# Kernel tuning notes

Hardware: AMD Instinct MI355X
Metric: run time of the kernel (lower is better)

## Reference

```python
import jax, jax.numpy as jnp
import numpy as np
from jax import lax

# Dimensions: B=batch, C=in_channels(=shells, shallow deep=0), O=out_channels,
# G=12 group orientations, (X,Y,Z)=volume, (H,W)=icosahedral chart plane.
B, C, O, G = 1, 8, 8, 12
X = 12
CH, CW = 8, 40  # chart height H and width 5*H (5 charts)


def setup_inputs() -> dict:
    key = jax.random.key(0)
    k1, k2, k3, k4 = jax.random.split(key, 4)
    x = jax.random.normal(k1, (B, C, X, X, X, CH, CW), jnp.float32)
    weight = 0.1 * jax.random.normal(k2, (O, C, 3, 3, 3, 7), jnp.float32)
    bias = 0.1 * jax.random.normal(k3, (O, 3, 3, 3), jnp.float32)
    # d12.basis_expansion (detached constant): 7 hex coeffs -> 12 oriented 3x3 kernels
    basis_e_h = jax.random.normal(k4, (G, 7, 3, 3), jnp.float32)
    # d12.padding_basis(H): chart-padding index maps. Interior = identity;
    # border ring gathers from adjacent-chart interior with orientation permutation.
    ys = jnp.arange(CH)
    xs = jnp.arange(CW)
    I = jnp.broadcast_to(jnp.clip(ys, 1, CH - 2)[:, None], (CH, CW)).astype(jnp.int32)
    J = jnp.broadcast_to(jnp.clip(xs, 1, CW - 2)[None, :], (CH, CW)).astype(jnp.int32)
    border = (ys[:, None] == 0) | (ys[:, None] == CH - 1) | (xs[None, :] == 0) | (xs[None, :] == CW - 1)
    g = jnp.arange(G)[:, None, None]
    T = jnp.where(border[None], (g + 1) % G, g).astype(jnp.int32)
    # d12.bias_basis: broadcast O biases over 12 orientations (g-major channel layout)
    bias_basis = jnp.tile(jnp.arange(O), G).astype(jnp.int32)
    return dict(x=x, weight=weight, bias=bias, basis_e_h=basis_e_h, I=I, J=J, T=T, bias_basis=bias_basis)


def _forward(x, weight, bias, basis_e_h, I, J, T, bias_basis):
    B, C, X, Y, Z, H, W = x.shape
    O = weight.shape[0]
    G = basis_e_h.shape[0]
    GO = G * O
    # Expand symmetry basis: per 3x3x3 offset, a [G*O, C, 3, 3] 2D kernel.
    kernel = jnp.einsum('ocijkb,gbuv->gocijkuv', weight, basis_e_h).reshape(GO, C, 3, 3, 3, 3, 3)
    # Original fills out[i+1] for i in range(X-3): Xo = X-3 valid positions (drops last).
    Xo, Yo, Zo = X - 3, Y - 3, Z - 3
    dn = ('NCHW', 'OIHW', 'NCHW')
    N = B * Xo * Yo * Zo
    acc = jnp.zeros((N, GO, H - 2, W - 2), x.dtype)
    # Sum over the 27 kernel offsets; each is a valid 3x3 conv2d on the chart plane.
    for fi in range(3):
        for fj in range(3):
            for fk in range(3):
                xs_ = x[:, :, fi:fi + Xo, fj:fj + Yo, fk:fk + Zo]  # [B,C,Xo,Yo,Zo,H,W]
                xs2 = xs_.transpose(0, 2, 3, 4, 1, 5, 6).reshape(N, C, H, W)
                acc = acc + lax.conv_general_dilated(xs2, kernel[:, :, fi, fj, fk], (1, 1), 'VALID', dimension_numbers=dn)
    # Sum of per-offset biases (bias added inside conv2d, before zero-pad ring).
    acc = acc + bias.sum(axis=(1, 2, 3))[bias_basis][None, :, None, None]
    acc = jnp.pad(acc, ((0, 0), (0, 0), (1, 1), (1, 1)))  # F.pad (1,1,1,1) -> [N,GO,H,W]
    # d12.pad: fill chart ring by gather with orientation permutation T.
    P = acc.reshape(N, G, O, H, W).transpose(0, 2, 1, 3, 4)  # [N,O,G,H,W]
    Ib = jnp.broadcast_to(I[None], (G, H, W))
    Jb = jnp.broadcast_to(J[None], (G, H, W))
    Pp = P[:, :, T, Ib, Jb]  # [N,O,G,H,W]
    res = Pp.transpose(0, 2, 1, 3, 4).reshape(B, Xo, Yo, Zo, GO, H, W).transpose(0, 4, 1, 2, 3, 5, 6)
    # Scatter into zero-initialized full volume at positions 1..X-3.
    out = jnp.zeros((B, GO, X, Y, Z, H, W), x.dtype)
    return out.at[:, :, 1:1 + Xo, 1:1 + Yo, 1:1 + Zo].set(res)


def reference(x, weight, bias, basis_e_h, I, J, T, bias_basis):
    return _forward(x, weight, bias, basis_e_h, I, J, T, bias_basis)
```

## Files before the change

### kernel.cpp

```cpp
#include <hip/hip_runtime.h>


#define HW 320
#define NZ 3
#define NPAD 1944

__global__ __launch_bounds__(320, 8) void fused_kernel(
    const float* __restrict__ x, const float* __restrict__ weight,
    const float* __restrict__ bias, const float* __restrict__ basis,
    float* __restrict__ out)
{
    __shared__ float qs[NZ * 7 * HW];

    const int tid = threadIdx.x;

    {
        float4* out4 = (float4*)out;
        const float4 z = make_float4(0.f, 0.f, 0.f, 0.f);
        for (int s = blockIdx.x * 320 + tid; s < 96 * 1728 * 80; s += NPAD * 320) {
            int row = s / 80;
            int xyz = row - (row / 1728) * 1728;
            int xi = xyz / 144;
            int r2 = xyz - xi * 144;
            int yi = r2 / 12;
            int zi = r2 - yi * 12;
            if (!((unsigned)(xi - 1) < 9u && (unsigned)(yi - 1) < 9u &&
                  (unsigned)(zi - 1) < 9u))
                out4[s] = z;
        }
    }

    const int xcd  = blockIdx.x & 7;
    const int slot = blockIdx.x >> 3;
    const int logical = xcd * (NPAD / 8) + slot;

    const int ntri = logical >> 3;
    const int o0   = logical & 7;
    const int xo = ntri / 27;
    const int rem = ntri - xo * 27;
    const int yo = rem / 3;
    const int zo = (rem - yo * 3) * NZ;

    float acc[NZ * 7];
    #pragma unroll
    for (int i = 0; i < NZ * 7; ++i) acc[i] = 0.f;

    const float* xb = x + ((xo * 12 + yo) * 12 + zo) * HW + tid;

    #pragma unroll 1
    for (int c = 0; c < 8; ++c) {
        const float* xc = xb + c * 1728 * HW;
        const float* wc = weight + o0 * 1512 + c * 189;
        #pragma unroll
        for (int fi = 0; fi < 3; ++fi) {
            #pragma unroll
            for (int fj = 0; fj < 3; ++fj) {
                float xv[NZ + 2];
                #pragma unroll
                for (int k5 = 0; k5 < NZ + 2; ++k5)
                    xv[k5] = xc[(fi * 144 + fj * 12 + k5) * HW];
                #pragma unroll
                for (int fk = 0; fk < 3; ++fk) {
                    const float* wp = wc + fi * 63 + fj * 21 + fk * 7;
                    #pragma unroll
                    for (int b = 0; b < 7; ++b) {
                        const float wv = wp[b];
                        #pragma unroll
                        for (int dz = 0; dz < NZ; ++dz)
                            acc[dz * 7 + b] = fmaf(xv[dz + fk], wv, acc[dz * 7 + b]);
                    }
                }
            }
        }
    }

    #pragma unroll
    for (int i = 0; i < NZ * 7; ++i) qs[i * HW + tid] = acc[i];
    __syncthreads();

    const int h = tid / 40;
    const int w = tid - h * 40;
    const int ii = min(max(h, 1), 6) - 1;
    const int jj = min(max(w, 1), 38) - 1;
    const bool border = (h == 0) | (h == 7) | (w == 0) | (w == 39);
    const int base_hw = ii * 40 + jj;

    float bs = 0.f;
    #pragma unroll
    for (int i = 0; i < 27; ++i) bs += bias[o0 * 27 + i];

    #pragma unroll 1
    for (int dz = 0; dz < NZ; ++dz) {
        float s[12];
        #pragma unroll
        for (int g = 0; g < 12; ++g) s[g] = 0.f;

        #pragma unroll 1
        for (int b = 0; b < 7; ++b) {
            float qw[9];
            #pragma unroll
            for (int uv = 0; uv < 9; ++uv) {
                const int u = uv / 3, v = uv - (uv / 3) * 3;
                qw[uv] = qs[(dz * 7 + b) * HW + base_hw + u * 40 + v];
            }
            const float* bb = basis + b * 9;
            #pragma unroll
            for (int g = 0; g < 12; ++g)
                #pragma unroll
                for (int uv = 0; uv < 9; ++uv)
                    s[g] = fmaf(qw[uv], bb[g * 63 + uv], s[g]);
        }

        const int out_xyz = ((xo + 1) * 144 + (yo + 1) * 12 + (zo + dz + 1)) * HW + tid;
        #pragma unroll
        for (int g = 0; g < 12; ++g) {
            float val = (border ? s[(g + 1) % 12] : s[g]) + bs;
            out[(g * 8 + o0) * (1728 * HW) + out_xyz] = val;
        }
    }
}

extern "C" void kernel_launch(void* const* d_in, const int* in_sizes, int n_in,
                              void* d_out, int out_size, void* d_ws, size_t ws_size,
                              hipStream_t stream)
{
    const float* x      = (const float*)d_in[0];
    const float* weight = (const float*)d_in[1];
    const float* bias   = (const float*)d_in[2];
    const float* basis  = (const float*)d_in[3];
    float* out = (float*)d_out;

    fused_kernel<<<NPAD, 320, 0, stream>>>(x, weight, bias, basis, out);
}
```

Before: 354.9 us.

## Compute all eight output channels per block instead of three z positions

Each block now handles one (x,y,z) output position and all 8 output channels, in place of one channel across 3 z positions. Each loaded x value is reused across 8 channels rather than across overlapping z windows. The grid shrinks from 1944 to 729 blocks and the XCD-aware block remapping is dropped. The 56-element accumulator raises register pressure, so launch bounds fall to 4 blocks per SM, and the basis stage runs in two shared-memory passes with an extra barrier.

```diff
diff --git a/kernel.cpp b/kernel.cpp
--- a/kernel.cpp
+++ b/kernel.cpp
@@ -2,22 +2,22 @@
 
 
 #define HW 320
-#define NZ 3
-#define NPAD 1944
+#define NB 729
 
-__global__ __launch_bounds__(320, 8) void fused_kernel(
+__global__ __launch_bounds__(320, 4) void fused_kernel(
     const float* __restrict__ x, const float* __restrict__ weight,
     const float* __restrict__ bias, const float* __restrict__ basis,
     float* __restrict__ out)
 {
-    __shared__ float qs[NZ * 7 * HW];
+    __shared__ float qs[4 * 7 * HW];
 
     const int tid = threadIdx.x;
 
     {
         float4* out4 = (float4*)out;
         const float4 z = make_float4(0.f, 0.f, 0.f, 0.f);
-        for (int s = blockIdx.x * 320 + tid; s < 96 * 1728 * 80; s += NPAD * 320) {
+        #pragma unroll 1
+        for (int s = blockIdx.x * 320 + tid; s < 96 * 1728 * 80; s += NB * 320) {
             int row = s / 80;
             int xyz = row - (row / 1728) * 1728;
             int xi = xyz / 144;
@@ -30,53 +30,42 @@
         }
     }
 
-    const int xcd  = blockIdx.x & 7;
-    const int slot = blockIdx.x >> 3;
-    const int logical = xcd * (NPAD / 8) + slot;
+    const int n  = blockIdx.x;
+    const int xo = n / 81;
+    const int rem = n - xo * 81;
+    const int yo = rem / 9;
+    const int zo = rem - yo * 9;
 
-    const int ntri = logical >> 3;
-    const int o0   = logical & 7;
-    const int xo = ntri / 27;
-    const int rem = ntri - xo * 27;
-    const int yo = rem / 3;
-    const int zo = (rem - yo * 3) * NZ;
-
-    float acc[NZ * 7];
+    float acc[56];
     #pragma unroll
-    for (int i = 0; i < NZ * 7; ++i) acc[i] = 0.f;
+    for (int i = 0; i < 56; ++i) acc[i] = 0.f;
 
     const float* xb = x + ((xo * 12 + yo) * 12 + zo) * HW + tid;
 
     #pragma unroll 1
     for (int c = 0; c < 8; ++c) {
-        const float* xc = xb + c * 1728 * HW;
-        const float* wc = weight + o0 * 1512 + c * 189;
+        const float* xc  = xb + c * 1728 * HW;
+        const float* wcb = weight + c * 189;
         #pragma unroll
         for (int fi = 0; fi < 3; ++fi) {
             #pragma unroll
             for (int fj = 0; fj < 3; ++fj) {
-                float xv[NZ + 2];
+                float xv[3];
                 #pragma unroll
-                for (int k5 = 0; k5 < NZ + 2; ++k5)
-                    xv[k5] = xc[(fi * 144 + fj * 12 + k5) * HW];
+                for (int fk = 0; fk < 3; ++fk)
+                    xv[fk] = xc[(fi * 144 + fj * 12 + fk) * HW];
                 #pragma unroll
-                for (int fk = 0; fk < 3; ++fk) {
-                    const float* wp = wc + fi * 63 + fj * 21 + fk * 7;
+                for (int o = 0; o < 8; ++o) {
+                    const float* wp = wcb + o * 1512 + fi * 63 + fj * 21;
                     #pragma unroll
-                    for (int b = 0; b < 7; ++b) {
-                        const float wv = wp[b];
+                    for (int fk = 0; fk < 3; ++fk)
                         #pragma unroll
-                        for (int dz = 0; dz < NZ; ++dz)
-                            acc[dz * 7 + b] = fmaf(xv[dz + fk], wv, acc[dz * 7 + b]);
-                    }
+                        for (int b = 0; b < 7; ++b)
+                            acc[o * 7 + b] = fmaf(xv[fk], wp[fk * 7 + b], acc[o * 7 + b]);
                 }
             }
         }
     }
-
-    #pragma unroll
-    for (int i = 0; i < NZ * 7; ++i) qs[i * HW + tid] = acc[i];
-    __syncthreads();
 
     const int h = tid / 40;
     const int w = tid - h * 40;
@@ -84,38 +73,48 @@
     const int jj = min(max(w, 1), 38) - 1;
     const bool border = (h == 0) | (h == 7) | (w == 0) | (w == 39);
     const int base_hw = ii * 40 + jj;
+    const int out_xyz = ((xo + 1) * 144 + (yo + 1) * 12 + (zo + 1)) * HW + tid;
 
-    float bs = 0.f;
     #pragma unroll
-    for (int i = 0; i < 27; ++i) bs += bias[o0 * 27 + i];
-
-    #pragma unroll 1
-    for (int dz = 0; dz < NZ; ++dz) {
-        float s[12];
+    for (int p = 0; p < 2; ++p) {
+        if (p) __syncthreads();
         #pragma unroll
-        for (int g = 0; g < 12; ++g) s[g] = 0.f;
+        for (int i = 0; i < 28; ++i)
+            qs[i * HW + tid] = acc[p * 28 + i];
+        __syncthreads();
 
         #pragma unroll 1
-        for (int b = 0; b < 7; ++b) {
-            float qw[9];
+        for (int oo = 0; oo < 4; ++oo) {
+            const int o = p * 4 + oo;
+            float sv[12];
             #pragma unroll
-            for (int uv = 0; uv < 9; ++uv) {
-                const int u = uv / 3, v = uv - (uv / 3) * 3;
-                qw[uv] = qs[(dz * 7 + b) * HW + base_hw + u * 40 + v];
+            for (int g = 0; g < 12; ++g) sv[g] = 0.f;
+
+            #pragma unroll 1
+            for (int b = 0; b < 7; ++b) {
+                float qw[9];
+                #pragma unroll
+                for (int uv = 0; uv < 9; ++uv) {
+                    const int u = uv / 3, v = uv - (uv / 3) * 3;
+                    qw[uv] = qs[(oo * 7 + b) * HW + base_hw + u * 40 + v];
+                }
+                const float* bb = basis + b * 9;
+                #pragma unroll
+                for (int g = 0; g < 12; ++g)
+                    #pragma unroll
+                    for (int uv = 0; uv < 9; ++uv)
+                        sv[g] = fmaf(qw[uv], bb[g * 63 + uv], sv[g]);
             }
-            const float* bb = basis + b * 9;
+
+            float bs = 0.f;
             #pragma unroll
-            for (int g = 0; g < 12; ++g)
-                #pragma unroll
-                for (int uv = 0; uv < 9; ++uv)
-                    s[g] = fmaf(qw[uv], bb[g * 63 + uv], s[g]);
-        }
+            for (int i = 0; i < 27; ++i) bs += bias[o * 27 + i];
 
-        const int out_xyz = ((xo + 1) * 144 + (yo + 1) * 12 + (zo + dz + 1)) * HW + tid;
-        #pragma unroll
-        for (int g = 0; g < 12; ++g) {
-            float val = (border ? s[(g + 1) % 12] : s[g]) + bs;
-            out[(g * 8 + o0) * (1728 * HW) + out_xyz] = val;
+            #pragma unroll
+            for (int g = 0; g < 12; ++g) {
+                float val = (border ? sv[(g + 1) % 12] : sv[g]) + bs;
+                out[(g * 8 + o) * (1728 * HW) + out_xyz] = val;
+            }
         }
     }
 }
@@ -130,5 +129,5 @@
     const float* basis  = (const float*)d_in[3];
     float* out = (float*)d_out;
 
-    fused_kernel<<<NPAD, 320, 0, stream>>>(x, weight, bias, basis, out);
+    fused_kernel<<<NB, 320, 0, stream>>>(x, weight, bias, basis, out);
 }
```

New measurement: 695.2 us. +95.9%, slower.
